# Optimization experiments

Measured on AMD Instinct MI355X. Metric: run time of the kernel, lower is better.

Reference implementation:

```python
import jax, jax.numpy as jnp
import numpy as np

B, T, D, E = 4, 2048, 1024, 8


def setup_inputs() -> dict:
    key = jax.random.key(0)
    ks = jax.random.split(key, 8)
    scale_g = float(np.sqrt(2.0 / (D + E)))  # xavier_uniform-ish scale for W_g
    scale_w = float(1.0 / np.sqrt(D))
    return {
        "x": jax.random.normal(ks[0], (B, T, D), dtype=jnp.float32),
        "noise": jax.random.normal(ks[1], (B, T, E), dtype=jnp.float32),  # the N(0,1) sample in Gating.forward
        "W_g": jax.random.normal(ks[2], (D, E), dtype=jnp.float32) * scale_g,
        "W_noise": jax.random.normal(ks[3], (D, E), dtype=jnp.float32),
        "W1": jax.random.normal(ks[4], (E, D, D), dtype=jnp.float32) * scale_w,
        "b1": jnp.zeros((E, D), dtype=jnp.float32),
        "W2": jax.random.normal(ks[5], (E, D, D), dtype=jnp.float32) * scale_w,
        "b2": jnp.zeros((E, D), dtype=jnp.float32),
        "k": 2,
    }


def _gates(x, noise, W_g, W_noise, k):
    # h = x@W_g + N(0,1) + softplus(x@W_noise)   (note: noise added, not scaled)
    h = jnp.einsum("btd,de->bte", x, W_g) + noise + jax.nn.softplus(
        jnp.einsum("btd,de->bte", x, W_noise)
    )
    kth = jax.lax.top_k(h, k)[0][..., -1:]           # kth largest per token
    h_masked = jnp.where(h >= kth, h, -jnp.inf)       # keepTopK (ties kept, as in torch)
    return jax.nn.softmax(h_masked, axis=-1)          # [B,T,E]


def reference(x, noise, W_g, W_noise, W1, b1, W2, b2, k):
    gates = _gates(x, noise, W_g, W_noise, k)
    # Dense loop over experts (faithful to original): every expert FFN on all tokens.
    # hidden: [E,B,T,D]
    hidden = jax.nn.relu(jnp.einsum("btd,edh->ebth", x, W1) + b1[:, None, None, :])
    expert_out = jnp.einsum("ebth,eho->ebto", hidden, W2) + b2[:, None, None, :]
    # mask-weighted combine: sum_e expert_out_e * gates[...,e]
    return jnp.einsum("ebtd,bte->btd", expert_out, gates)
```

## Files before the change

kernel.cpp:

```cpp
#include <hip/hip_runtime.h>
#include <hip/hip_bf16.h>

#define BTOK 8192
#define DDIM 1024
#define NEXP 8

typedef unsigned short u16;
typedef unsigned int u32;
typedef __attribute__((ext_vector_type(8))) short short8;
typedef __attribute__((ext_vector_type(4))) float f32x4;

constexpr int BM = 256, BN = 256, BK = 64;
constexpr int SLOTCAP = 3072;
constexpr int NT = DDIM / BK;

__device__ __forceinline__ u16 f2bf(float f){
  __hip_bfloat16 h = __float2bfloat16(f);
  return *reinterpret_cast<u16*>(&h);
}
__device__ __forceinline__ float bf2f(u16 v){
  return __uint_as_float(((u32)v) << 16);
}
__device__ __forceinline__ void gll16(const u16* gsrc, u16* ldst){
  __builtin_amdgcn_global_load_lds((const __attribute__((address_space(1))) void*)gsrc,
                                   (__attribute__((address_space(3))) void*)ldst,
                                   16, 0, 0);
}

__global__ __launch_bounds__(256) void cast_x_kernel(const float4* __restrict__ x4,
                                                     ushort4* __restrict__ xb4)
{
  const int i = blockIdx.x*256 + threadIdx.x;
  const float4 v = x4[i];
  xb4[i] = make_ushort4(f2bf(v.x), f2bf(v.y), f2bf(v.z), f2bf(v.w));
}

__global__ __launch_bounds__(256) void wprep_kernel(
    const float* __restrict__ Wg, const float* __restrict__ Wn,
    u16* __restrict__ wpt)
{
  const int idx = blockIdx.x*256 + threadIdx.x;
  const int n = idx >> 10, d = idx & 1023;
  const float v = (n < 8) ? Wg[d*8 + n] : Wn[d*8 + (n-8)];
  const u16 hi = f2bf(v);
  const u16 lo = f2bf(v - bf2f(hi));
  wpt[n*1024 + d]          = hi;
  wpt[16384 + n*1024 + d]  = lo;
}

__global__ __launch_bounds__(128) void score_kernel(
    const float* __restrict__ x, const u16* __restrict__ xb,
    const u16* __restrict__ wpt, float* __restrict__ hp)
{
  __shared__ __align__(16) u16 lw[2][16][1024];
  const int tid = threadIdx.x;
  const int wave = tid >> 6, lane = tid & 63;

  for (int it = 0; it < 32; ++it){
    const int cid = it*128 + tid;
    const int v = cid >> 11, rem = cid & 2047;
    const int n = rem >> 7, c = rem & 127;
    const short8 val = *reinterpret_cast<const short8*>(wpt + v*16384 + n*1024 + c*8);
    *reinterpret_cast<short8*>(&lw[v][n][(c ^ (n&7))*8]) = val;
  }
  __syncthreads();

  const int q = lane >> 4, l16 = lane & 15;
  const int t0 = blockIdx.x*32 + wave*16;
  const int rowA = t0 + l16;
  const u16*   xbp = xb + (size_t)rowA*DDIM + q*8;
  const float* xp  = x  + (size_t)rowA*DDIM + q*8;

  f32x4 acc0 = {0.f,0.f,0.f,0.f}, acc1 = acc0, acc2 = acc0;
  for (int kt = 0; kt < 32; ++kt){
    const short8 ah = *reinterpret_cast<const short8*>(xbp + kt*32);
    const float4 x0 = *reinterpret_cast<const float4*>(xp + kt*32);
    const float4 x1 = *reinterpret_cast<const float4*>(xp + kt*32 + 4);
    short8 al;
    al[0]=(short)f2bf(x0.x - bf2f((u16)ah[0])); al[1]=(short)f2bf(x0.y - bf2f((u16)ah[1]));
    al[2]=(short)f2bf(x0.z - bf2f((u16)ah[2])); al[3]=(short)f2bf(x0.w - bf2f((u16)ah[3]));
    al[4]=(short)f2bf(x1.x - bf2f((u16)ah[4])); al[5]=(short)f2bf(x1.y - bf2f((u16)ah[5]));
    al[6]=(short)f2bf(x1.z - bf2f((u16)ah[6])); al[7]=(short)f2bf(x1.w - bf2f((u16)ah[7]));
    const int bs = ((kt*4 + q) ^ (l16 & 7)) * 8;
    const short8 bh = *reinterpret_cast<const short8*>(&lw[0][l16][bs]);
    const short8 bl = *reinterpret_cast<const short8*>(&lw[1][l16][bs]);
    acc0 = __builtin_amdgcn_mfma_f32_16x16x32_bf16(ah, bh, acc0, 0, 0, 0);
    acc1 = __builtin_amdgcn_mfma_f32_16x16x32_bf16(al, bh, acc1, 0, 0, 0);
    acc2 = __builtin_amdgcn_mfma_f32_16x16x32_bf16(ah, bl, acc2, 0, 0, 0);
  }
  #pragma unroll
  for (int r = 0; r < 4; ++r)
    hp[(size_t)(t0 + q*4 + r)*16 + l16] = acc0[r] + acc1[r] + acc2[r];
}

__global__ __launch_bounds__(256) void gating_select_kernel(
    const float* __restrict__ hp, const float* __restrict__ noise,
    const int* __restrict__ kp,
    float* __restrict__ gates, int* __restrict__ counts, int* __restrict__ lists,
    int* __restrict__ tokmap, int* __restrict__ ncnt)
{
  __shared__ int lcnt[NEXP];
  __shared__ int lbase[NEXP];
  const int tid = threadIdx.x;
  const int t   = blockIdx.x*256 + tid;
  if (tid < NEXP) lcnt[tid] = 0;
  __syncthreads();

  float hg[16];
  #pragma unroll
  for (int i = 0; i < 4; ++i){
    const float4 v = reinterpret_cast<const float4*>(hp + (size_t)t*16)[i];
    hg[i*4+0]=v.x; hg[i*4+1]=v.y; hg[i*4+2]=v.z; hg[i*4+3]=v.w;
  }
  float h[NEXP];
  #pragma unroll
  for (int e = 0; e < NEXP; ++e){
    const float hn = hg[8+e];
    const float sp = (hn > 20.f) ? hn : log1pf(expf(hn));
    h[e] = hg[e] + noise[(size_t)t*NEXP + e] + sp;
  }

  int kk = *kp; kk = kk<1?1:(kk>NEXP?NEXP:kk);
  bool used[NEXP];
  #pragma unroll
  for (int e=0;e<NEXP;e++) used[e]=false;
  float kth = 0.f;
  for (int i=0;i<kk;i++){
    int bi=0; float bv=-3.4e38f;
    #pragma unroll
    for (int e=0;e<NEXP;e++) if (!used[e] && h[e]>bv){bv=h[e]; bi=e;}
    used[bi]=true; kth=bv;
  }
  float m=-3.4e38f;
  #pragma unroll
  for (int e=0;e<NEXP;e++) if (h[e]>=kth && h[e]>m) m=h[e];
  float p[NEXP], s=0.f;
  #pragma unroll
  for (int e=0;e<NEXP;e++){ p[e]=(h[e]>=kth)?expf(h[e]-m):0.f; s+=p[e]; }
  const float inv = 1.f/s;
  float g[NEXP];
  int lslot[NEXP];
  #pragma unroll
  for (int e=0;e<NEXP;e++){
    g[e] = p[e]*inv;
    gates[(size_t)t*NEXP + e] = g[e];
    if (g[e] > 0.f) lslot[e] = atomicAdd(&lcnt[e], 1);
  }
  __syncthreads();
  if (tid < NEXP) lbase[tid] = atomicAdd(&counts[tid], lcnt[tid]);
  __syncthreads();
  int idx = 0;
  #pragma unroll
  for (int e=0;e<NEXP;e++){
    if (g[e] > 0.f){
      const int slot = lbase[e] + lslot[e];
      lists[e*BTOK + slot] = t;
      tokmap[t*NEXP + idx] = (e << 13) | (slot & 8191);
      idx++;
    }
  }
  ncnt[t] = idx;
}

__global__ __launch_bounds__(256) void trans_kernel(
    const float* __restrict__ W1, const float* __restrict__ W2,
    u16* __restrict__ W1T, u16* __restrict__ W2T)
{
  __shared__ float tile[64][65];
  const int mz = blockIdx.z;
  const float* src = (mz < NEXP) ? (W1  + (size_t)mz*DDIM*DDIM) : (W2  + (size_t)(mz-NEXP)*DDIM*DDIM);
  u16*       dst = (mz < NEXP) ? (W1T + (size_t)mz*DDIM*DDIM) : (W2T + (size_t)(mz-NEXP)*DDIM*DDIM);
  const int r0 = blockIdx.x*64, c0 = blockIdx.y*64;
  const int tx = threadIdx.x & 63, ty = threadIdx.x >> 6;
  #pragma unroll
  for (int i=ty;i<64;i+=4)
    tile[i][tx] = src[(size_t)(r0+i)*DDIM + c0+tx];
  __syncthreads();
  #pragma unroll
  for (int i=ty;i<64;i+=4)
    dst[(size_t)(c0+i)*DDIM + r0+tx] = f2bf(tile[tx][i]);
}

template<int LAYER>
__device__ __forceinline__ void ffn_body(
    const u16* __restrict__ Asrc, const u16* __restrict__ WT,
    const float* __restrict__ bias,
    const int* __restrict__ counts, const int* __restrict__ lists,
    u16* __restrict__ dst)
{
  const int lin = blockIdx.x;
  const int e   = lin & 7;
  const int idx = lin >> 3;
  const int m0  = (idx >> 2) * BM;
  const int n0  = (idx & 3)  * BN;
  int cnt = counts[e]; if (cnt > SLOTCAP) cnt = SLOTCAP;
  if (m0 >= cnt) return;

  __shared__ __align__(16) u16 ldsA[2][BM*BK];
  __shared__ __align__(16) u16 ldsB[2][BN*BK];

  const int tid = threadIdx.x;
  const int wave = tid>>6, lane = tid&63;
  const int wm = wave>>2, wn = wave&3;

  const u16* aSrc[4]; const u16* bSrc[4];
  {
    const int lr = lane>>3, sp = lane&7;
    #pragma unroll
    for (int i=0;i<4;i++){
      const int row = wave*32 + i*8 + lr;
      const int ku  = sp ^ (row&7);
      size_t abase;
      if constexpr (LAYER==1){
        int gr = m0 + row; if (gr >= cnt) gr = cnt-1;
        abase = (size_t)lists[e*BTOK + gr] * DDIM;
      } else {
        abase = ((size_t)e*SLOTCAP + m0 + row) * DDIM;
      }
      aSrc[i] = Asrc + abase + ku*8;
      bSrc[i] = WT + ((size_t)e*DDIM + n0 + row)*DDIM + ku*8;
    }
  }

  const int q = lane>>4, l16 = lane&15;
  int aoff[8], boff[4];
  #pragma unroll
  for (int f=0;f<8;f++){
    const int ra = wm*128 + f*16 + l16;
    aoff[f] = ra*BK + ((q ^ (ra&7))*8);
  }
  #pragma unroll
  for (int f=0;f<4;f++){
    const int rb = wn*64 + f*16 + l16;
    boff[f] = rb*BK + ((q ^ (rb&7))*8);
  }

  f32x4 acc[8][4];
  #pragma unroll
  for (int i=0;i<8;i++)
    #pragma unroll
    for (int j=0;j<4;j++)
      acc[i][j] = (f32x4){0.f,0.f,0.f,0.f};

  #define STAGE(T, c)                                            \
    _Pragma("unroll")                                            \
    for (int i=0;i<4;i++){                                       \
      gll16(aSrc[i] + (size_t)(T)*BK, &ldsA[c][(wave*32+i*8)*BK]); \
      gll16(bSrc[i] + (size_t)(T)*BK, &ldsB[c][(wave*32+i*8)*BK]); \
    }

  STAGE(0, 0)
  STAGE(1, 1)
  asm volatile("s_waitcnt vmcnt(8)" ::: "memory");
  __builtin_amdgcn_sched_barrier(0);
  __builtin_amdgcn_s_barrier();
  __builtin_amdgcn_sched_barrier(0);

  for (int kt = 0; kt < NT; ++kt){
    const int c = kt & 1;
    #pragma unroll
    for (int kk=0; kk<2; kk++){
      const int kx = kk ? 32 : 0;
      short8 bfr[4], afr[8];
      #pragma unroll
      for (int f=0;f<4;f++) bfr[f] = *reinterpret_cast<const short8*>(&ldsB[c][boff[f] ^ kx]);
      #pragma unroll
      for (int f=0;f<8;f++) afr[f] = *reinterpret_cast<const short8*>(&ldsA[c][aoff[f] ^ kx]);
      __builtin_amdgcn_s_setprio(1);
      #pragma unroll
      for (int fm=0;fm<8;fm++)
        #pragma unroll
        for (int fn=0;fn<4;fn++)
          acc[fm][fn] = __builtin_amdgcn_mfma_f32_16x16x32_bf16(afr[fm], bfr[fn], acc[fm][fn], 0, 0, 0);
      __builtin_amdgcn_s_setprio(0);
    }
    __builtin_amdgcn_sched_barrier(0);
    __builtin_amdgcn_s_barrier();
    __builtin_amdgcn_sched_barrier(0);
    if (kt + 2 < NT){
      STAGE(kt+2, c)
      asm volatile("s_waitcnt vmcnt(8)" ::: "memory");
    } else {
      asm volatile("s_waitcnt vmcnt(0)" ::: "memory");
    }
    __builtin_amdgcn_sched_barrier(0);
    __builtin_amdgcn_s_barrier();
    __builtin_amdgcn_sched_barrier(0);
  }
  #undef STAGE

  #pragma unroll
  for (int fm=0;fm<8;fm++){
    #pragma unroll
    for (int r=0;r<4;r++){
      const int row = wm*128 + fm*16 + q*4 + r;
      const int gr  = m0 + row;
      #pragma unroll
      for (int fn=0;fn<4;fn++){
        const int col = n0 + wn*64 + fn*16 + l16;
        float v = acc[fm][fn][r] + bias[e*DDIM + col];
        if constexpr (LAYER==1) v = v > 0.f ? v : 0.f;
        dst[((size_t)e*SLOTCAP + gr)*DDIM + col] = f2bf(v);
      }
    }
  }
}

__global__ __launch_bounds__(512, 1) void ffn1_kernel(
    const u16* __restrict__ A, const u16* __restrict__ WT, const float* __restrict__ b,
    const int* __restrict__ counts, const int* __restrict__ lists, u16* __restrict__ dst)
{ ffn_body<1>(A, WT, b, counts, lists, dst); }

__global__ __launch_bounds__(512, 1) void ffn2_kernel(
    const u16* __restrict__ A, const u16* __restrict__ WT, const float* __restrict__ b,
    const int* __restrict__ counts, const int* __restrict__ lists, u16* __restrict__ dst)
{ ffn_body<2>(A, WT, b, counts, lists, dst); }

__global__ __launch_bounds__(256) void combine_kernel(
    const u16* __restrict__ partial, const int* __restrict__ tokmap,
    const int* __restrict__ ncnt, const float* __restrict__ gates,
    float* __restrict__ out)
{
  const int t = blockIdx.x, c = threadIdx.x;
  const int n = ncnt[t];
  float4 acc = {0.f, 0.f, 0.f, 0.f};
  for (int j = 0; j < n; ++j){
    const int ent  = tokmap[t*NEXP + j];
    const int e    = ent >> 13, slot = ent & 8191;
    if (slot >= SLOTCAP) continue;
    const float g = gates[(size_t)t*NEXP + e];
    const ushort4 pv = reinterpret_cast<const ushort4*>(
        partial + ((size_t)e*SLOTCAP + slot)*DDIM)[c];
    acc.x = fmaf(g, bf2f(pv.x), acc.x);
    acc.y = fmaf(g, bf2f(pv.y), acc.y);
    acc.z = fmaf(g, bf2f(pv.z), acc.z);
    acc.w = fmaf(g, bf2f(pv.w), acc.w);
  }
  reinterpret_cast<float4*>(out + (size_t)t*DDIM)[c] = acc;
}

extern "C" void kernel_launch(void* const* d_in, const int* in_sizes, int n_in,
                              void* d_out, int out_size, void* d_ws, size_t ws_size,
                              hipStream_t stream)
{
  const float* x     = (const float*)d_in[0];
  const float* noise = (const float*)d_in[1];
  const float* Wg    = (const float*)d_in[2];
  const float* Wn    = (const float*)d_in[3];
  const float* W1    = (const float*)d_in[4];
  const float* b1    = (const float*)d_in[5];
  const float* W2    = (const float*)d_in[6];
  const float* b2    = (const float*)d_in[7];
  const int*   kp    = (const int*)d_in[8];
  float* out = (float*)d_out;

  char* ws = (char*)d_ws;
  int*   counts = (int*)ws;
  int*   lists  = (int*)(ws + 4096);
  float* gates  = (float*)(ws + 266240);
  int*   tokmap = (int*)(ws + 528384);
  int*   ncnt   = (int*)(ws + 790528);
  u16*   xb     = (u16*)(ws + 823296);
  u16*   W1T    = (u16*)(ws + 17600512);
  u16*   W2T    = (u16*)(ws + 34377728);
  u16*   hidden = (u16*)(ws + 51154944);
  u16*   partial= (u16*)(ws + 101486592);
  float* hp     = (float*)(ws + 101486592);
  u16*   wpt    = (u16*)(ws + 102010880);
  const size_t NEED = 151818240ull;

  hipMemsetAsync(counts, 0, 64, stream);
  if (ws_size < NEED){
    hipMemsetAsync(d_out, 0, (size_t)out_size*sizeof(float), stream);
    return;
  }

  cast_x_kernel<<<BTOK*DDIM/4/256, 256, 0, stream>>>((const float4*)x, (ushort4*)xb);
  wprep_kernel<<<64, 256, 0, stream>>>(Wg, Wn, wpt);
  trans_kernel<<<dim3(16,16,16), 256, 0, stream>>>(W1, W2, W1T, W2T);
  score_kernel<<<BTOK/32, 128, 0, stream>>>(x, xb, wpt, hp);
  gating_select_kernel<<<BTOK/256, 256, 0, stream>>>(hp, noise, kp, gates, counts, lists,
                                                     tokmap, ncnt);
  ffn1_kernel<<<(SLOTCAP/BM)*4*NEXP, 512, 0, stream>>>(
      xb, W1T, b1, counts, lists, hidden);
  ffn2_kernel<<<(SLOTCAP/BM)*4*NEXP, 512, 0, stream>>>(
      hidden, W2T, b2, counts, lists, partial);
  combine_kernel<<<BTOK, 256, 0, stream>>>(partial, tokmap, ncnt, gates, out);
}
```

Baseline: 328.2 us.

## Fuse x bf16 cast into score kernel and simplify FFN pipeline sync

Removes the separate cast_x kernel; score_kernel now converts x to bf16 in registers and writes xb, saving one launch and a full read of x plus a read of xb. Separately, the FFN GEMM main loop drops its explicit vmcnt waits and split barriers in favour of a prefetch-next-then-__syncthreads double buffer. The new loop issues the next tile's loads at the top of each iteration and relies on __syncthreads to order LDS writes, which may change how much load latency is hidden and whether the compiler inserts conservative waits.

```diff
diff --git a/kernel.cpp b/kernel.cpp
--- a/kernel.cpp
+++ b/kernel.cpp
@@ -25,14 +25,6 @@
   __builtin_amdgcn_global_load_lds((const __attribute__((address_space(1))) void*)gsrc,
                                    (__attribute__((address_space(3))) void*)ldst,
                                    16, 0, 0);
-}
-
-__global__ __launch_bounds__(256) void cast_x_kernel(const float4* __restrict__ x4,
-                                                     ushort4* __restrict__ xb4)
-{
-  const int i = blockIdx.x*256 + threadIdx.x;
-  const float4 v = x4[i];
-  xb4[i] = make_ushort4(f2bf(v.x), f2bf(v.y), f2bf(v.z), f2bf(v.w));
 }
 
 __global__ __launch_bounds__(256) void wprep_kernel(
@@ -49,8 +41,8 @@
 }
 
 __global__ __launch_bounds__(128) void score_kernel(
-    const float* __restrict__ x, const u16* __restrict__ xb,
-    const u16* __restrict__ wpt, float* __restrict__ hp)
+    const float* __restrict__ x, const u16* __restrict__ wpt,
+    float* __restrict__ hp, u16* __restrict__ xb)
 {
   __shared__ __align__(16) u16 lw[2][16][1024];
   const int tid = threadIdx.x;
@@ -68,14 +60,19 @@
   const int q = lane >> 4, l16 = lane & 15;
   const int t0 = blockIdx.x*32 + wave*16;
   const int rowA = t0 + l16;
-  const u16*   xbp = xb + (size_t)rowA*DDIM + q*8;
   const float* xp  = x  + (size_t)rowA*DDIM + q*8;
+  u16*         xbo = xb + (size_t)rowA*DDIM + q*8;
 
   f32x4 acc0 = {0.f,0.f,0.f,0.f}, acc1 = acc0, acc2 = acc0;
   for (int kt = 0; kt < 32; ++kt){
-    const short8 ah = *reinterpret_cast<const short8*>(xbp + kt*32);
     const float4 x0 = *reinterpret_cast<const float4*>(xp + kt*32);
     const float4 x1 = *reinterpret_cast<const float4*>(xp + kt*32 + 4);
+    short8 ah;
+    ah[0]=(short)f2bf(x0.x); ah[1]=(short)f2bf(x0.y);
+    ah[2]=(short)f2bf(x0.z); ah[3]=(short)f2bf(x0.w);
+    ah[4]=(short)f2bf(x1.x); ah[5]=(short)f2bf(x1.y);
+    ah[6]=(short)f2bf(x1.z); ah[7]=(short)f2bf(x1.w);
+    *reinterpret_cast<short8*>(xbo + kt*32) = ah;
     short8 al;
     al[0]=(short)f2bf(x0.x - bf2f((u16)ah[0])); al[1]=(short)f2bf(x0.y - bf2f((u16)ah[1]));
     al[2]=(short)f2bf(x0.z - bf2f((u16)ah[2])); al[3]=(short)f2bf(x0.w - bf2f((u16)ah[3]));
@@ -250,22 +247,18 @@
     }
 
   STAGE(0, 0)
-  STAGE(1, 1)
-  asm volatile("s_waitcnt vmcnt(8)" ::: "memory");
-  __builtin_amdgcn_sched_barrier(0);
-  __builtin_amdgcn_s_barrier();
-  __builtin_amdgcn_sched_barrier(0);
-
+  __syncthreads();
+  int cur = 0;
   for (int kt = 0; kt < NT; ++kt){
-    const int c = kt & 1;
+    if (kt + 1 < NT) STAGE(kt+1, cur^1)
     #pragma unroll
     for (int kk=0; kk<2; kk++){
       const int kx = kk ? 32 : 0;
       short8 bfr[4], afr[8];
       #pragma unroll
-      for (int f=0;f<4;f++) bfr[f] = *reinterpret_cast<const short8*>(&ldsB[c][boff[f] ^ kx]);
+      for (int f=0;f<4;f++) bfr[f] = *reinterpret_cast<const short8*>(&ldsB[cur][boff[f] ^ kx]);
       #pragma unroll
-      for (int f=0;f<8;f++) afr[f] = *reinterpret_cast<const short8*>(&ldsA[c][aoff[f] ^ kx]);
+      for (int f=0;f<8;f++) afr[f] = *reinterpret_cast<const short8*>(&ldsA[cur][aoff[f] ^ kx]);
       __builtin_amdgcn_s_setprio(1);
       #pragma unroll
       for (int fm=0;fm<8;fm++)
@@ -274,18 +267,8 @@
           acc[fm][fn] = __builtin_amdgcn_mfma_f32_16x16x32_bf16(afr[fm], bfr[fn], acc[fm][fn], 0, 0, 0);
       __builtin_amdgcn_s_setprio(0);
     }
-    __builtin_amdgcn_sched_barrier(0);
-    __builtin_amdgcn_s_barrier();
-    __builtin_amdgcn_sched_barrier(0);
-    if (kt + 2 < NT){
-      STAGE(kt+2, c)
-      asm volatile("s_waitcnt vmcnt(8)" ::: "memory");
-    } else {
-      asm volatile("s_waitcnt vmcnt(0)" ::: "memory");
-    }
-    __builtin_amdgcn_sched_barrier(0);
-    __builtin_amdgcn_s_barrier();
-    __builtin_amdgcn_sched_barrier(0);
+    __syncthreads();
+    cur ^= 1;
   }
   #undef STAGE
 
@@ -375,10 +358,9 @@
     return;
   }
 
-  cast_x_kernel<<<BTOK*DDIM/4/256, 256, 0, stream>>>((const float4*)x, (ushort4*)xb);
   wprep_kernel<<<64, 256, 0, stream>>>(Wg, Wn, wpt);
   trans_kernel<<<dim3(16,16,16), 256, 0, stream>>>(W1, W2, W1T, W2T);
-  score_kernel<<<BTOK/32, 128, 0, stream>>>(x, xb, wpt, hp);
+  score_kernel<<<BTOK/32, 128, 0, stream>>>(x, wpt, hp, xb);
   gating_select_kernel<<<BTOK/256, 256, 0, stream>>>(hp, noise, kp, gates, counts, lists,
                                                      tokmap, ncnt);
   ffn1_kernel<<<(SLOTCAP/BM)*4*NEXP, 512, 0, stream>>>(
```

Result: no change. 324.0 us (-1.3%).
